# Kernel tuning notes

Hardware: AMD Instinct MI355X
Metric: run time of the kernel (lower is better)

The kernel has to match this reference:

```python
import jax, jax.numpy as jnp
import numpy as np

TAU = 10.0          # tau_init
R_MAX = 8           # max(groupconvs)
GROUPCONVS = (4, 8)
PADS = (0, 8)       # (k - spat_red)//2 for k in (17, 33), spat_red = 33 - 2*8 = 17
NEG_SLOPE = 0.01    # LeakyReLU default


def lrelu(t):
    return jnp.where(t >= 0, t, NEG_SLOPE * t)


def rotate_kernel(w, theta):
    """Rotate square kernels w:[N,k,k] by theta, matching torch
    F.affine_grid + F.grid_sample (bilinear, zero padding, align_corners=False)."""
    N, k, _ = w.shape
    coords = (2.0 * jnp.arange(k) + 1.0) / k - 1.0  # normalized pixel centers
    gy, gx = jnp.meshgrid(coords, coords, indexing='ij')
    c, s = jnp.cos(theta), jnp.sin(theta)
    sx = c * gx - s * gy
    sy = s * gx + c * gy
    fx = ((sx + 1.0) * k - 1.0) / 2.0
    fy = ((sy + 1.0) * k - 1.0) / 2.0
    x0 = jnp.floor(fx).astype(jnp.int32)
    y0 = jnp.floor(fy).astype(jnp.int32)
    wf = w.reshape(N, k * k)

    def gather(yi, xi):
        valid = ((yi >= 0) & (yi < k) & (xi >= 0) & (xi < k)).astype(w.dtype)
        idx = jnp.clip(yi, 0, k - 1) * k + jnp.clip(xi, 0, k - 1)
        return wf[:, idx.reshape(-1)].reshape(N, k, k) * valid

    wx1 = fx - x0
    wy1 = fy - y0
    return (gather(y0, x0) * (1 - wy1) * (1 - wx1)
            + gather(y0, x0 + 1) * (1 - wy1) * wx1
            + gather(y0 + 1, x0) * wy1 * (1 - wx1)
            + gather(y0 + 1, x0 + 1) * wy1 * wx1)


def group_conv(x, w, b, pad):
    """GroupConv with input_rot_dim=1: x [B,1,H,W], w [O,1,1,k,k] -> [B,O,R_MAX,H',W']."""
    O, k = w.shape[0], w.shape[-1]
    w2 = w.reshape(O, k, k)
    angles = (2.0 * jnp.pi / R_MAX) * jnp.arange(R_MAX)
    tw = jax.vmap(lambda th: rotate_kernel(w2, th))(angles)   # [R,O,k,k]
    tw = jnp.transpose(tw, (1, 0, 2, 3)).reshape(O * R_MAX, 1, k, k)
    y = jax.lax.conv_general_dilated(x, tw, (1, 1), [(pad, pad), (pad, pad)],
                                     dimension_numbers=('NCHW', 'OIHW', 'NCHW'))
    B, _, H, W = y.shape
    return y.reshape(B, O, R_MAX, H, W) + b[None, :, None, None, None]


def conv1x1(h, w, b):
    # 1x1x1 Conv3d: h [B,C,R,H,W], w [O,C], b [O]
    return jnp.einsum('bcrhw,oc->borhw', h, w) + b[None, :, None, None, None]


def scatter_sum(outs, weights, axis):
    """slice_scatter-based alignment: embed smaller-rdim tensors into the
    largest one at stride max_dim//dim, weight, and sum."""
    max_out = outs[-1]
    md = max_out.shape[axis]
    total = max_out * weights[-1]
    for i, o in enumerate(outs[:-1]):
        step = md // o.shape[axis]
        idx = tuple(slice(None, None, step) if a == axis else slice(None)
                    for a in range(max_out.ndim))
        total = total + jnp.zeros_like(max_out).at[idx].set(o) * weights[i]
    return total


OFFSETS = np.array([0, np.pi / 4, np.pi / 2, 3 * np.pi / 4, np.pi,
                    -3 * np.pi / 4, -np.pi / 2, -np.pi / 4], dtype=np.float32)


def _forward(x, ksize_weight, rdim_weight, conv1_w0, conv1_b0, conv1_w1, conv1_b1,
             conv2_w, conv2_b, conva_w, conva_b, convz_w, convz_b,
             g_ksize, g_rdim, g_attn):
    # gumbel-softmax over kernel sizes (soft, tau=TAU)
    alphas = jax.nn.softmax((ksize_weight + g_ksize) / TAU)
    x_out = (alphas[0] * lrelu(group_conv(x, conv1_w0, conv1_b0, PADS[0]))
             + alphas[1] * lrelu(group_conv(x, conv1_w1, conv1_b1, PADS[1])))
    xs_out = [x_out[:, :, ::R_MAX // r] for r in GROUPCONVS]
    hs = [lrelu(conv1x1(xo, conv2_w[i], conv2_b[i])) for i, xo in enumerate(xs_out)]
    attns = [conv1x1(h, conva_w[i], conva_b[i])[:, 0] for i, h in enumerate(hs)]
    betas = jax.nn.softmax((rdim_weight + g_rdim) / TAU)
    attn = scatter_sum(attns, betas, axis=1)          # [B,R,H,W]
    offsets = jnp.asarray(OFFSETS)
    sigma = np.pi  # theta_prior; Normal(0, sigma) log-prob at offsets
    p_r = (-0.5 * (offsets / sigma) ** 2 - np.float32(np.log(sigma))
           - np.float32(0.5 * np.log(2.0 * np.pi)))[:, None, None]
    attn = attn + p_r
    B = attn.shape[0]
    flat = attn.reshape(B, -1)
    q_t_r = jax.nn.log_softmax(flat, axis=1).reshape(attn.shape)
    # F.gumbel_softmax(a, dim=-1) with default tau=1
    a_sampled = jax.nn.softmax(flat + g_attn, axis=-1).reshape(attn.shape)
    zs = [conv1x1(h, convz_w[i], convz_b[i]) for i, h in enumerate(hs)]
    z = scatter_sum(zs, betas, axis=2)                # [B,2L,R,H,W]
    # faithful to source: `thetas = [c_r(h) for c_r, h in zip(self.conv_z, hs)]`
    # reuses conv_z, so pre-refinement theta == z
    theta_pre = z
    rotation_offset = jnp.broadcast_to(offsets[None, :, None, None], a_sampled.shape)
    theta = jnp.stack((theta_pre[:, 0] + rotation_offset, theta_pre[:, 1]), axis=1)
    return attn, q_t_r, p_r, a_sampled, offsets, theta, z


def setup_inputs() -> dict:
    key = jax.random.key(0)
    ks = jax.random.split(key, 16)
    B, n, KN, L = 8, 64, 128, 2
    gum = lambda k, shape: -jnp.log(-jnp.log(
        jax.random.uniform(k, shape, jnp.float32, 1e-10, 1.0)))
    return {
        'x': jax.random.normal(ks[0], (B, 1, n, n), jnp.float32),
        'ksize_weight': 0.001 * jax.random.normal(ks[1], (2,), jnp.float32),
        'rdim_weight': 0.001 * jax.random.normal(ks[2], (2,), jnp.float32),
        'conv1_w0': 0.02 * jax.random.normal(ks[3], (KN, 1, 1, 17, 17), jnp.float32),
        'conv1_b0': 0.01 * jax.random.normal(ks[4], (KN,), jnp.float32),
        'conv1_w1': 0.02 * jax.random.normal(ks[5], (KN, 1, 1, 33, 33), jnp.float32),
        'conv1_b1': 0.01 * jax.random.normal(ks[6], (KN,), jnp.float32),
        'conv2_w': (1.0 / np.sqrt(KN)) * jax.random.normal(ks[7], (2, KN, KN), jnp.float32),
        'conv2_b': 0.01 * jax.random.normal(ks[8], (2, KN), jnp.float32),
        'conva_w': (1.0 / np.sqrt(KN)) * jax.random.normal(ks[9], (2, 1, KN), jnp.float32),
        'conva_b': 0.01 * jax.random.normal(ks[10], (2, 1), jnp.float32),
        'convz_w': (1.0 / np.sqrt(KN)) * jax.random.normal(ks[11], (2, 2 * L, KN), jnp.float32),
        'convz_b': 0.01 * jax.random.normal(ks[12], (2, 2 * L), jnp.float32),
        'g_ksize': gum(ks[13], (2,)),
        'g_rdim': gum(ks[14], (2,)),
        'g_attn': gum(ks[15], (B, R_MAX * 48 * 48)),
    }


def reference(x, ksize_weight, rdim_weight, conv1_w0, conv1_b0, conv1_w1, conv1_b1,
              conv2_w, conv2_b, conva_w, conva_b, convz_w, convz_b,
              g_ksize, g_rdim, g_attn):
    return _forward(x, ksize_weight, rdim_weight, conv1_w0, conv1_b0, conv1_w1,
                    conv1_b1, conv2_w, conv2_b, conva_w, conva_b, convz_w, convz_b,
                    g_ksize, g_rdim, g_attn)
```

## Files before the change

### kernel.cpp

```cpp
#include <hip/hip_runtime.h>
#include <hip/hip_bf16.h>
#include <math.h>

#define PI_D 3.14159265358979323846

typedef __attribute__((ext_vector_type(8))) short bf16x8;
typedef __attribute__((ext_vector_type(4))) float f32x4;

#define OFF_SCAL   0u
#define OFF_W2B    4u
#define OFF_BF     16388u
#define OFF_XOUTB  917508u
#define OFF_A0     10354692u
#define OFF_A1     10428420u
#define OFF_Z0     10575876u
#define OFF_Z1     10870788u

#define NS33 42
#define NS17 13

__device__ __forceinline__ float off_r(int r) {
  int m = (r <= 4) ? r : r - 8;
  return (float)(PI_D / 4.0) * (float)m;
}
__device__ __forceinline__ float lrelu_f(float v) { return (v >= 0.f) ? v : 0.01f * v; }
__device__ __forceinline__ short f2bf(float f) {
  __bf16 h = (__bf16)f;
  return __builtin_bit_cast(short, h);
}

__global__ void k_prep(const float* __restrict__ kw, const float* __restrict__ gk,
                       const float* __restrict__ rw, const float* __restrict__ gr,
                       const float* __restrict__ w0, const float* __restrict__ w1,
                       const float* __restrict__ w2, float* __restrict__ scal,
                       short* __restrict__ w2b, short* __restrict__ bfrag) {
  int t = blockIdx.x * blockDim.x + threadIdx.x;
  if (t == 0) {
    float a0 = (kw[0] + gk[0]) * 0.1f, a1 = (kw[1] + gk[1]) * 0.1f;
    float m = fmaxf(a0, a1);
    float e0 = expf(a0 - m), e1 = expf(a1 - m), inv = 1.f / (e0 + e1);
    scal[0] = e0 * inv; scal[1] = e1 * inv;
    float b0 = (rw[0] + gr[0]) * 0.1f, b1 = (rw[1] + gr[1]) * 0.1f;
    m = fmaxf(b0, b1);
    e0 = expf(b0 - m); e1 = expf(b1 - m); inv = 1.f / (e0 + e1);
    scal[2] = e0 * inv; scal[3] = e1 * inv;
  }
  if (t < 2 * 128 * 128) w2b[t] = f2bf(w2[t]);
  int o = t & 127;
  int q = t >> 7;
  int kb = q & 3; q >>= 2;
  int c = q % 55; int r = q / 55;
  float theta = (float)(PI_D / 4.0) * (float)r;
  float cth = cosf(theta), sth = sinf(theta);
  short out[8];
#pragma unroll
  for (int j = 0; j < 8; ++j) {
    float val = 0.f;
    int kk, k, dy, dx;
    const float* wsrc;
    if (c < NS33) { kk = 32 * c + 8 * kb + j; k = 33; dy = kk / 40; dx = kk - 40 * dy; wsrc = w1; }
    else          { kk = 32 * (c - NS33) + 8 * kb + j; k = 17; dy = kk / 24; dx = kk - 24 * dy; wsrc = w0; }
    if (dy < k && dx < k) {
      int kk2 = k * k;
      const float* wo = wsrc + o * kk2;
      float cy = (2.0f * (float)dy + 1.0f) / (float)k - 1.0f;
      float cx = (2.0f * (float)dx + 1.0f) / (float)k - 1.0f;
      float sx = cth * cx - sth * cy;
      float sy = sth * cx + cth * cy;
      float fx = ((sx + 1.0f) * (float)k - 1.0f) * 0.5f;
      float fy = ((sy + 1.0f) * (float)k - 1.0f) * 0.5f;
      float x0f = floorf(fx), y0f = floorf(fy);
      int x0 = (int)x0f, y0 = (int)y0f;
      float wx1 = fx - x0f, wy1 = fy - y0f;
      float acc = 0.f;
#define CORNER(Y, X, CW) { int yy = (Y), xx = (X); \
      if (yy >= 0 && yy < k && xx >= 0 && xx < k) acc += wo[yy * k + xx] * (CW); }
      CORNER(y0,     x0,     (1.f - wy1) * (1.f - wx1));
      CORNER(y0,     x0 + 1, (1.f - wy1) * wx1);
      CORNER(y0 + 1, x0,     wy1 * (1.f - wx1));
      CORNER(y0 + 1, x0 + 1, wy1 * wx1);
#undef CORNER
      val = acc;
    }
    out[j] = f2bf(val);
  }
  *(bf16x8*)(bfrag + (size_t)t * 8) =
      (bf16x8){out[0], out[1], out[2], out[3], out[4], out[5], out[6], out[7]};
}

#define TDW 3080
#define PADW 26
__global__ __launch_bounds__(256, 4) void k_conv_mfma(
    const float* __restrict__ x, const short* __restrict__ bfrag,
    const float* __restrict__ b17, const float* __restrict__ b33,
    const float* __restrict__ scal, short* __restrict__ xoutb) {
  __shared__ __align__(16) float tile[TDW + PADW + TDW];
  float* tB = tile + (TDW + PADW);
  int blk = blockIdx.x;
  int pt = blk % 36; int t2 = blk / 36; int r = t2 & 7, b = t2 >> 3;
  int p0 = pt * 64;
  int ybase = p0 / 48;
  int tid = threadIdx.x;
  for (int idx = tid; idx < TDW; idx += 256) {
    int ty = idx / 88, tx = idx - ty * 88;
    int gy = ybase + ty - 8, gx = tx - 8;
    float v = 0.f;
    if (gy >= 0 && gy < 64 && gx >= 0 && gx < 64) v = x[(b * 64 + gy) * 64 + gx];
    tile[idx] = v;
    if (idx > 0) tB[idx - 1] = v;
  }
  for (int idx = tid; idx < PADW; idx += 256) tile[TDW + idx] = 0.f;
  if (tid == 0) tB[TDW - 1] = 0.f;
  __syncthreads();

  int lane = tid & 63, w = tid >> 6;
  int wm = w >> 1, wn = w & 1;
  int kc = lane >> 4;
  int ln = lane & 15;
  int mloc[2];
#pragma unroll
  for (int mf = 0; mf < 2; ++mf) {
    int p = p0 + wm * 32 + mf * 16 + ln;
    int ym = p / 48, xm = p - ym * 48;
    mloc[mf] = (ym - ybase) * 88 + xm;
  }
  const short* bb = bfrag + (size_t)r * (55 * 4 * 128 * 8);
  int nb0 = wn * 64;

  f32x4 acc33[2][4];
#pragma unroll
  for (int mf = 0; mf < 2; ++mf)
#pragma unroll
    for (int nf = 0; nf < 4; ++nf) acc33[mf][nf] = (f32x4){0.f, 0.f, 0.f, 0.f};

#define LOADB(dst, cg)                                                          \
  {                                                                             \
    _Pragma("unroll")                                                           \
    for (int nf = 0; nf < 4; ++nf)                                              \
      dst[nf] = *(const bf16x8*)(bb + ((size_t)((cg)*4 + kc) * 128 + nb0 + nf * 16 + ln) * 8); \
  }
#define READA(dst, vv)                                                          \
  {                                                                             \
    int s_ = (vv) & 1;                                                          \
    const float2* pp_ = (const float2*)(tile + s_ * (TDW + PADW) + ((vv) & ~1));\
    float2 f0_ = pp_[0], f1_ = pp_[1], f2_ = pp_[2], f3_ = pp_[3];              \
    dst = (bf16x8){f2bf(f0_.x), f2bf(f0_.y), f2bf(f1_.x), f2bf(f1_.y),          \
                   f2bf(f2_.x), f2bf(f2_.y), f2bf(f3_.x), f2bf(f3_.y)};         \
  }

  {
    int dxb = 8 * kc;
    int off = dxb;
    bf16x8 bc[4], bn[4];
    LOADB(bc, 0);
    for (int c = 0; c < NS33; ++c) {
      if (c + 1 < NS33) LOADB(bn, c + 1);
      bf16x8 a0, a1;
      READA(a0, mloc[0] + off);
      READA(a1, mloc[1] + off);
#pragma unroll
      for (int nf = 0; nf < 4; ++nf) {
        acc33[0][nf] = __builtin_amdgcn_mfma_f32_16x16x32_bf16(a0, bc[nf], acc33[0][nf], 0, 0, 0);
        acc33[1][nf] = __builtin_amdgcn_mfma_f32_16x16x32_bf16(a1, bc[nf], acc33[1][nf], 0, 0, 0);
      }
#pragma unroll
      for (int nf = 0; nf < 4; ++nf) bc[nf] = bn[nf];
      int nd = dxb + 32;
      int wr = (nd >= 40);
      dxb = wr ? nd - 40 : nd;
      off += wr ? 80 : 32;
    }
  }

  f32x4 acc17[2][4];
#pragma unroll
  for (int mf = 0; mf < 2; ++mf)
#pragma unroll
    for (int nf = 0; nf < 4; ++nf) acc17[mf][nf] = (f32x4){0.f, 0.f, 0.f, 0.f};
  {
    int t8 = 8 * kc;
    int dy0 = t8 / 24;
    int dxb = t8 - 24 * dy0;
    int off = (8 + dy0) * 88 + 8 + dxb;
    for (int c = 0; c < NS17; ++c) {
      bf16x8 bc[4];
      LOADB(bc, NS33 + c);
      bf16x8 a0, a1;
      READA(a0, mloc[0] + off);
      READA(a1, mloc[1] + off);
#pragma unroll
      for (int nf = 0; nf < 4; ++nf) {
        acc17[0][nf] = __builtin_amdgcn_mfma_f32_16x16x32_bf16(a0, bc[nf], acc17[0][nf], 0, 0, 0);
        acc17[1][nf] = __builtin_amdgcn_mfma_f32_16x16x32_bf16(a1, bc[nf], acc17[1][nf], 0, 0, 0);
      }
      int nd = dxb + 8;
      int wr = (nd >= 24);
      dxb = wr ? nd - 24 : nd;
      off += wr ? 160 : 96;
    }
  }
#undef LOADB
#undef READA

  float a0s = scal[0], a1s = scal[1];
  int dq = lane >> 4;
#pragma unroll
  for (int nf = 0; nf < 4; ++nf) {
    int n = nb0 + nf * 16 + ln;
    float bb17 = b17[n], bb33 = b33[n];
#pragma unroll
    for (int mf = 0; mf < 2; ++mf) {
#pragma unroll
      for (int i = 0; i < 4; ++i) {
        int m = wm * 32 + mf * 16 + dq * 4 + i;
        float v = a0s * lrelu_f(acc17[mf][nf][i] + bb17)
                + a1s * lrelu_f(acc33[mf][nf][i] + bb33);
        xoutb[((size_t)(b * 8 + r) * 2304 + p0 + m) * 128 + n] = f2bf(v);
      }
    }
  }
}

__global__ __launch_bounds__(256, 8) void k_pw_mfma(
    const short* __restrict__ xoutb, const short* __restrict__ w2b_,
    const float* __restrict__ b2_, const float* __restrict__ wa_,
    const float* __restrict__ ba_, const float* __restrict__ wz_,
    const float* __restrict__ bz_,
    float* __restrict__ a0buf, float* __restrict__ z0buf,
    float* __restrict__ a1buf, float* __restrict__ z1buf) {
  int blk = blockIdx.x;
  int i1 = (blk >= 1152);
  int lblk = i1 ? blk - 1152 : blk;
  int nR = i1 ? 8 : 4, rstep = i1 ? 1 : 2;
  const short* w2b = w2b_ + (i1 ? 128 * 128 : 0);
  const float* b2 = b2_ + (i1 ? 128 : 0);
  const float* wa = wa_ + (i1 ? 128 : 0);
  const float* ba = ba_ + i1;
  const float* wz = wz_ + (i1 ? 512 : 0);
  const float* bz = bz_ + (i1 ? 4 : 0);
  float* attn_out = i1 ? a1buf : a0buf;
  float* z_out = i1 ? z1buf : z0buf;

  int pblk = lblk % 36;
  int t = lblk / 36;
  int rl = t % nR;
  int b = t / nR;
  int tid = threadIdx.x;
  int lane = tid & 63, w = tid >> 6;
  int kc = lane >> 4, ln = lane & 15;
  int pwave = pblk * 64 + w * 16;
  const short* arow = xoutb + ((size_t)(b * 8 + rl * rstep) * 2304 + pwave) * 128;

  f32x4 acc[8];
#pragma unroll
  for (int nf = 0; nf < 8; ++nf) acc[nf] = (f32x4){0.f, 0.f, 0.f, 0.f};
#pragma unroll
  for (int s = 0; s < 4; ++s) {
    bf16x8 a = *(const bf16x8*)(arow + ln * 128 + s * 32 + kc * 8);
#pragma unroll
    for (int nf = 0; nf < 8; ++nf) {
      bf16x8 bv = *(const bf16x8*)(w2b + (nf * 16 + ln) * 128 + s * 32 + kc * 8);
      acc[nf] = __builtin_amdgcn_mfma_f32_16x16x32_bf16(a, bv, acc[nf], 0, 0, 0);
    }
  }

  float attn_acc[4] = {0.f, 0.f, 0.f, 0.f};
  float zacc[4][4];
#pragma unroll
  for (int j = 0; j < 4; ++j)
#pragma unroll
    for (int q = 0; q < 4; ++q) zacc[j][q] = 0.f;
#pragma unroll
  for (int nf = 0; nf < 8; ++nf) {
    int n = nf * 16 + ln;
    float bb2 = b2[n];
    float wan = wa[n];
    float wz0 = wz[n], wz1 = wz[128 + n], wz2 = wz[256 + n], wz3 = wz[384 + n];
#pragma unroll
    for (int q = 0; q < 4; ++q) {
      float h = lrelu_f(acc[nf][q] + bb2);
      attn_acc[q] = fmaf(wan, h, attn_acc[q]);
      zacc[0][q] = fmaf(wz0, h, zacc[0][q]);
      zacc[1][q] = fmaf(wz1, h, zacc[1][q]);
      zacc[2][q] = fmaf(wz2, h, zacc[2][q]);
      zacc[3][q] = fmaf(wz3, h, zacc[3][q]);
    }
  }
#pragma unroll
  for (int off = 1; off < 16; off <<= 1) {
#pragma unroll
    for (int q = 0; q < 4; ++q) {
      attn_acc[q] += __shfl_xor(attn_acc[q], off);
#pragma unroll
      for (int j = 0; j < 4; ++j) zacc[j][q] += __shfl_xor(zacc[j][q], off);
    }
  }
  if (ln == 0) {
    float ba0 = ba[0];
#pragma unroll
    for (int q = 0; q < 4; ++q) {
      int pix = pwave + kc * 4 + q;
      attn_out[((size_t)b * nR + rl) * 2304 + pix] = attn_acc[q] + ba0;
#pragma unroll
      for (int j = 0; j < 4; ++j)
        z_out[(((size_t)b * 4 + j) * nR + rl) * 2304 + pix] = zacc[j][q] + bz[j];
    }
  }
}

__global__ void k_attn_combine(const float* __restrict__ a0buf, const float* __restrict__ a1buf,
                               const float* __restrict__ scal, float* __restrict__ out0,
                               float* __restrict__ out2, float* __restrict__ out4) {
  int idx = blockIdx.x * blockDim.x + threadIdx.x;
  if (idx < 8) {
    float off = off_r(idx);
    out4[idx] = off;
    float q = off / (float)PI_D;
    out2[idx] = -0.5f * q * q - logf((float)PI_D) - 0.5f * logf(2.0f * (float)PI_D);
  }
  if (idx >= 147456) return;
  int pix = idx % 2304;
  int t = idx / 2304;
  int r = t & 7, b = t >> 3;
  float v = scal[3] * a1buf[idx];
  if (!(r & 1)) v += scal[2] * a0buf[((size_t)b * 4 + (r >> 1)) * 2304 + pix];
  float q = off_r(r) / (float)PI_D;
  v += -0.5f * q * q - logf((float)PI_D) - 0.5f * logf(2.0f * (float)PI_D);
  out0[idx] = v;
}

__global__ __launch_bounds__(1024) void k_softmax(const float* __restrict__ out0,
                                                  const float* __restrict__ g,
                                                  float* __restrict__ out1,
                                                  float* __restrict__ out3) {
  int b = blockIdx.x;
  int tid = threadIdx.x;
  const float* v = out0 + (size_t)b * 18432;
  const float* gb = g + (size_t)b * 18432;
  float vl[18], gl[18];
  float m1 = -1e30f, m2 = -1e30f;
#pragma unroll
  for (int t = 0; t < 18; ++t) {
    float vv = v[tid + (t << 10)];
    float gg = gb[tid + (t << 10)];
    vl[t] = vv;
    gl[t] = vv + gg;
    m1 = fmaxf(m1, vv);
    m2 = fmaxf(m2, gl[t]);
  }
  __shared__ float red[32];
  for (int off = 32; off > 0; off >>= 1) {
    m1 = fmaxf(m1, __shfl_xor(m1, off));
    m2 = fmaxf(m2, __shfl_xor(m2, off));
  }
  int wid = tid >> 6, lane = tid & 63;
  if (lane == 0) { red[wid] = m1; red[wid + 16] = m2; }
  __syncthreads();
  float M1 = red[0], M2 = red[16];
#pragma unroll
  for (int w = 1; w < 16; ++w) { M1 = fmaxf(M1, red[w]); M2 = fmaxf(M2, red[w + 16]); }
  __syncthreads();
  float s1 = 0.f, s2 = 0.f;
#pragma unroll
  for (int t = 0; t < 18; ++t) { s1 += expf(vl[t] - M1); s2 += expf(gl[t] - M2); }
  for (int off = 32; off > 0; off >>= 1) {
    s1 += __shfl_xor(s1, off);
    s2 += __shfl_xor(s2, off);
  }
  if (lane == 0) { red[wid] = s1; red[wid + 16] = s2; }
  __syncthreads();
  float S1 = 0.f, S2 = 0.f;
#pragma unroll
  for (int w = 0; w < 16; ++w) { S1 += red[w]; S2 += red[w + 16]; }
  float lse = M1 + logf(S1);
  float inv2 = 1.0f / S2;
  float* o1 = out1 + (size_t)b * 18432;
  float* o3 = out3 + (size_t)b * 18432;
#pragma unroll
  for (int t = 0; t < 18; ++t) {
    o1[tid + (t << 10)] = vl[t] - lse;
    o3[tid + (t << 10)] = expf(gl[t] - M2) * inv2;
  }
}

__global__ void k_ztheta(const float* __restrict__ z0buf, const float* __restrict__ z1buf,
                         const float* __restrict__ scal, float* __restrict__ out5,
                         float* __restrict__ out6) {
  int idx = blockIdx.x * blockDim.x + threadIdx.x;
  if (idx >= 589824) return;
  int pix = idx % 2304;
  int t = idx / 2304;
  int r = t & 7;
  t >>= 3;
  int c = t & 3;
  int b = t >> 2;
  float v = scal[3] * z1buf[idx];
  if (!(r & 1)) v += scal[2] * z0buf[(((size_t)b * 4 + c) * 4 + (r >> 1)) * 2304 + pix];
  out6[idx] = v;
  if (c == 0)      out5[(((size_t)b * 2 + 0) * 8 + r) * 2304 + pix] = v + off_r(r);
  else if (c == 1) out5[(((size_t)b * 2 + 1) * 8 + r) * 2304 + pix] = v;
}

extern "C" void kernel_launch(void* const* d_in, const int* in_sizes, int n_in,
                              void* d_out, int out_size, void* d_ws, size_t ws_size,
                              hipStream_t stream) {
  const float* x   = (const float*)d_in[0];
  const float* ksz = (const float*)d_in[1];
  const float* rdw = (const float*)d_in[2];
  const float* w0  = (const float*)d_in[3];
  const float* b0  = (const float*)d_in[4];
  const float* w1  = (const float*)d_in[5];
  const float* b1  = (const float*)d_in[6];
  const float* w2  = (const float*)d_in[7];
  const float* b2  = (const float*)d_in[8];
  const float* wa  = (const float*)d_in[9];
  const float* ba  = (const float*)d_in[10];
  const float* wz  = (const float*)d_in[11];
  const float* bz  = (const float*)d_in[12];
  const float* gks = (const float*)d_in[13];
  const float* grd = (const float*)d_in[14];
  const float* gat = (const float*)d_in[15];
  float* out = (float*)d_out;
  float* ws  = (float*)d_ws;

  float* scal = ws + OFF_SCAL;
  short* w2b  = (short*)(ws + OFF_W2B);
  short* bfr  = (short*)(ws + OFF_BF);
  short* xoutb = (short*)(ws + OFF_XOUTB);
  float* a0b  = ws + OFF_A0;
  float* a1b  = ws + OFF_A1;
  float* z0b  = ws + OFF_Z0;
  float* z1b  = ws + OFF_Z1;

  float* out0 = out;
  float* out1 = out + 147456;
  float* out2 = out + 294912;
  float* out3 = out + 294920;
  float* out4 = out + 442376;
  float* out5 = out + 442384;
  float* out6 = out + 737296;

  k_prep<<<880, 256, 0, stream>>>(ksz, gks, rdw, grd, w0, w1, w2, scal, w2b, bfr);
  k_conv_mfma<<<2304, 256, 0, stream>>>(x, bfr, b0, b1, scal, xoutb);
  k_pw_mfma<<<3456, 256, 0, stream>>>(xoutb, w2b, b2, wa, ba, wz, bz,
                                      a0b, z0b, a1b, z1b);
  k_attn_combine<<<576, 256, 0, stream>>>(a0b, a1b, scal, out0, out2, out4);
  k_softmax<<<8, 1024, 0, stream>>>(out0, gat, out1, out3);
  k_ztheta<<<2304, 256, 0, stream>>>(z0b, z1b, scal, out5, out6);
}
```

Before: 314.0 us.

## Store conv input tile as bf16 with parity-split rows and coalesce pointwise outputs

The conv kernel now converts the input tile to bf16 once when filling LDS and stores it as two half-word-shifted copies. Each MFMA fragment becomes four 32-bit LDS loads bit-cast directly, with no per-iteration float-to-bf16 conversion. The M-row mapping is interleaved (even/odd pixels per fragment) so each fragment reads from a fixed parity buffer, and the output index mapping is changed to match. The pointwise kernel stages its attention and z results in shared memory and writes them with all 256 threads in coalesced rows, at the cost of an extra barrier.

```diff
diff --git a/kernel.cpp b/kernel.cpp
--- a/kernel.cpp
+++ b/kernel.cpp
@@ -6,6 +6,7 @@
 
 typedef __attribute__((ext_vector_type(8))) short bf16x8;
 typedef __attribute__((ext_vector_type(4))) float f32x4;
+typedef __attribute__((ext_vector_type(4))) unsigned int u32x4;
 
 #define OFF_SCAL   0u
 #define OFF_W2B    4u
@@ -89,13 +90,14 @@
 }
 
 #define TDW 3080
-#define PADW 26
+#define SHW 1544
 __global__ __launch_bounds__(256, 4) void k_conv_mfma(
     const float* __restrict__ x, const short* __restrict__ bfrag,
     const float* __restrict__ b17, const float* __restrict__ b33,
     const float* __restrict__ scal, short* __restrict__ xoutb) {
-  __shared__ __align__(16) float tile[TDW + PADW + TDW];
-  float* tB = tile + (TDW + PADW);
+  __shared__ unsigned int lds[SHW + 1540];
+  unsigned short* lA = (unsigned short*)lds;
+  unsigned short* lB = (unsigned short*)(lds + SHW);
   int blk = blockIdx.x;
   int pt = blk % 36; int t2 = blk / 36; int r = t2 & 7, b = t2 >> 3;
   int p0 = pt * 64;
@@ -106,11 +108,11 @@
     int gy = ybase + ty - 8, gx = tx - 8;
     float v = 0.f;
     if (gy >= 0 && gy < 64 && gx >= 0 && gx < 64) v = x[(b * 64 + gy) * 64 + gx];
-    tile[idx] = v;
-    if (idx > 0) tB[idx - 1] = v;
-  }
-  for (int idx = tid; idx < PADW; idx += 256) tile[TDW + idx] = 0.f;
-  if (tid == 0) tB[TDW - 1] = 0.f;
+    unsigned short h = (unsigned short)f2bf(v);
+    lA[idx] = h;
+    if (idx > 0) lB[idx - 1] = h;
+  }
+  if (tid == 0) lB[TDW - 1] = 0;
   __syncthreads();
 
   int lane = tid & 63, w = tid >> 6;
@@ -120,7 +122,7 @@
   int mloc[2];
 #pragma unroll
   for (int mf = 0; mf < 2; ++mf) {
-    int p = p0 + wm * 32 + mf * 16 + ln;
+    int p = p0 + wm * 32 + mf + 2 * ln;
     int ym = p / 48, xm = p - ym * 48;
     mloc[mf] = (ym - ybase) * 88 + xm;
   }
@@ -139,13 +141,11 @@
     for (int nf = 0; nf < 4; ++nf)                                              \
       dst[nf] = *(const bf16x8*)(bb + ((size_t)((cg)*4 + kc) * 128 + nb0 + nf * 16 + ln) * 8); \
   }
-#define READA(dst, vv)                                                          \
+#define READA(dst, mf, vv)                                                      \
   {                                                                             \
-    int s_ = (vv) & 1;                                                          \
-    const float2* pp_ = (const float2*)(tile + s_ * (TDW + PADW) + ((vv) & ~1));\
-    float2 f0_ = pp_[0], f1_ = pp_[1], f2_ = pp_[2], f3_ = pp_[3];              \
-    dst = (bf16x8){f2bf(f0_.x), f2bf(f0_.y), f2bf(f1_.x), f2bf(f1_.y),          \
-                   f2bf(f2_.x), f2bf(f2_.y), f2bf(f3_.x), f2bf(f3_.y)};         \
+    int bd_ = ((vv) >> 1) + ((mf) ? SHW : 0);                                   \
+    u32x4 uv_ = {lds[bd_], lds[bd_ + 1], lds[bd_ + 2], lds[bd_ + 3]};           \
+    dst = __builtin_bit_cast(bf16x8, uv_);                                      \
   }
 
   {
@@ -156,8 +156,8 @@
     for (int c = 0; c < NS33; ++c) {
       if (c + 1 < NS33) LOADB(bn, c + 1);
       bf16x8 a0, a1;
-      READA(a0, mloc[0] + off);
-      READA(a1, mloc[1] + off);
+      READA(a0, 0, mloc[0] + off);
+      READA(a1, 1, mloc[1] + off);
 #pragma unroll
       for (int nf = 0; nf < 4; ++nf) {
         acc33[0][nf] = __builtin_amdgcn_mfma_f32_16x16x32_bf16(a0, bc[nf], acc33[0][nf], 0, 0, 0);
@@ -186,8 +186,8 @@
       bf16x8 bc[4];
       LOADB(bc, NS33 + c);
       bf16x8 a0, a1;
-      READA(a0, mloc[0] + off);
-      READA(a1, mloc[1] + off);
+      READA(a0, 0, mloc[0] + off);
+      READA(a1, 1, mloc[1] + off);
 #pragma unroll
       for (int nf = 0; nf < 4; ++nf) {
         acc17[0][nf] = __builtin_amdgcn_mfma_f32_16x16x32_bf16(a0, bc[nf], acc17[0][nf], 0, 0, 0);
@@ -212,7 +212,7 @@
     for (int mf = 0; mf < 2; ++mf) {
 #pragma unroll
       for (int i = 0; i < 4; ++i) {
-        int m = wm * 32 + mf * 16 + dq * 4 + i;
+        int m = wm * 32 + mf + 8 * dq + 2 * i;
         float v = a0s * lrelu_f(acc17[mf][nf][i] + bb17)
                 + a1s * lrelu_f(acc33[mf][nf][i] + bb33);
         xoutb[((size_t)(b * 8 + r) * 2304 + p0 + m) * 128 + n] = f2bf(v);
@@ -228,6 +228,8 @@
     const float* __restrict__ bz_,
     float* __restrict__ a0buf, float* __restrict__ z0buf,
     float* __restrict__ a1buf, float* __restrict__ z1buf) {
+  __shared__ float sA[64];
+  __shared__ float sZ[4][64];
   int blk = blockIdx.x;
   int i1 = (blk >= 1152);
   int lblk = i1 ? blk - 1152 : blk;
@@ -245,10 +247,11 @@
   int t = lblk / 36;
   int rl = t % nR;
   int b = t / nR;
+  int pix0 = pblk * 64;
   int tid = threadIdx.x;
   int lane = tid & 63, w = tid >> 6;
   int kc = lane >> 4, ln = lane & 15;
-  int pwave = pblk * 64 + w * 16;
+  int pwave = pix0 + w * 16;
   const short* arow = xoutb + ((size_t)(b * 8 + rl * rstep) * 2304 + pwave) * 128;
 
   f32x4 acc[8];
@@ -299,13 +302,17 @@
     float ba0 = ba[0];
 #pragma unroll
     for (int q = 0; q < 4; ++q) {
-      int pix = pwave + kc * 4 + q;
-      attn_out[((size_t)b * nR + rl) * 2304 + pix] = attn_acc[q] + ba0;
-#pragma unroll
-      for (int j = 0; j < 4; ++j)
-        z_out[(((size_t)b * 4 + j) * nR + rl) * 2304 + pix] = zacc[j][q] + bz[j];
-    }
-  }
+      int px = w * 16 + kc * 4 + q;
+      sA[px] = attn_acc[q] + ba0;
+#pragma unroll
+      for (int j = 0; j < 4; ++j) sZ[j][px] = zacc[j][q] + bz[j];
+    }
+  }
+  __syncthreads();
+  int px = tid & 63, jj = tid >> 6;
+  if (jj == 0)
+    attn_out[((size_t)b * nR + rl) * 2304 + pix0 + px] = sA[px];
+  z_out[(((size_t)b * 4 + jj) * nR + rl) * 2304 + pix0 + px] = sZ[jj][px];
 }
 
 __global__ void k_attn_combine(const float* __restrict__ a0buf, const float* __restrict__ a1buf,
```

Result: no change. 316.3 us (+0.7%).
